# Optimization experiments

Hardware: AMD Instinct MI355X
Metric: run time of the kernel (lower is better)

## Reference

```python
import jax, jax.numpy as jnp
import numpy as np

N_USERS = 30000
N_ENT = 70000
N = N_USERS + N_ENT          # total graph nodes
E = 1_600_000                # edges (avg degree 16)
D = 64                       # embed_dim
B = 4096                     # scored user-item pairs
LEAKY_SLOPE = 0.01           # torch nn.LeakyReLU default
EPS = 1e-12                  # torch F.normalize default eps


def setup_inputs() -> dict:
    key = jax.random.key(0)
    ks = jax.random.split(key, 16)
    inp = {
        "edge_row": jax.random.randint(ks[0], (E,), 0, N, dtype=jnp.int32),
        "edge_col": jax.random.randint(ks[1], (E,), 0, N, dtype=jnp.int32),
        "edge_vals": jax.random.uniform(ks[2], (E,), dtype=jnp.float32) / 16.0,
        "user_embed": jax.random.normal(ks[3], (N_USERS, D), jnp.float32) * 0.1,
        "entity_embed": jax.random.normal(ks[4], (N_ENT, D), jnp.float32) * 0.1,
        "W1_0": jax.random.normal(ks[5], (D, 64), jnp.float32) * (1.0 / np.sqrt(D)),
        "b1_0": jnp.zeros((64,), jnp.float32),
        "W2_0": jax.random.normal(ks[6], (D, 64), jnp.float32) * (1.0 / np.sqrt(D)),
        "b2_0": jnp.zeros((64,), jnp.float32),
        "W1_1": jax.random.normal(ks[7], (64, 32), jnp.float32) * (1.0 / 8.0),
        "b1_1": jnp.zeros((32,), jnp.float32),
        "W2_1": jax.random.normal(ks[8], (64, 32), jnp.float32) * (1.0 / 8.0),
        "b2_1": jnp.zeros((32,), jnp.float32),
        "user_ids": jax.random.randint(ks[9], (B,), 0, N_USERS, dtype=jnp.int32),
        "item_ids": jax.random.randint(ks[10], (B,), 0, N_ENT, dtype=jnp.int32),
    }
    return inp


def _gnn_layer(feats, edge_row, edge_col, edge_vals, W1, b1, W2, b2):
    # sparse adj @ feats  ==  scatter-add of weighted source features to rows
    gathered = feats[edge_col] * edge_vals[:, None]          # (E, d_in)
    h_neigh = jax.ops.segment_sum(gathered, edge_row, num_segments=N)  # (N, d_in)
    term1 = (feats + h_neigh) @ W1 + b1
    term2 = (feats * h_neigh) @ W2 + b2
    h = jax.nn.leaky_relu(term1 + term2, negative_slope=LEAKY_SLOPE)
    # F.normalize(h, p=2, dim=1)
    norm = jnp.linalg.norm(h, axis=1, keepdims=True)
    return h / jnp.maximum(norm, EPS)


def reference(edge_row, edge_col, edge_vals, user_embed, entity_embed,
              W1_0, b1_0, W2_0, b2_0, W1_1, b1_1, W2_1, b2_1,
              user_ids, item_ids):
    a0 = jnp.concatenate([user_embed, entity_embed], axis=0)     # (N, 64)
    a1 = _gnn_layer(a0, edge_row, edge_col, edge_vals, W1_0, b1_0, W2_0, b2_0)  # (N, 64)
    a2 = _gnn_layer(a1, edge_row, edge_col, edge_vals, W1_1, b1_1, W2_1, b2_1)  # (N, 32)
    final = jnp.concatenate([a0, a1, a2], axis=1)                # (N, 160)
    u = final[user_ids]                                          # (B, 160)
    i = final[N_USERS + item_ids]                                # (B, 160)
    return jnp.sum(u * i, axis=1)                                # (B,)
```

## Files before the change

kernel.cpp:

```cpp
#include <hip/hip_runtime.h>
#include <hip/hip_bf16.h>
#include <math.h>

#define LEAKY 0.01f
#define SCAN_BLOCK 256
#define SCAN_ITEMS 4
#define SCAN_TILE (SCAN_BLOCK * SCAN_ITEMS)

struct __align__(8) Bf4 { __hip_bfloat16 a, b, c, d; };

__global__ void zero_i32(int* __restrict__ p, int n) {
    int i = blockIdx.x * blockDim.x + threadIdx.x;
    if (i < n) p[i] = 0;
}

__global__ void count_edges(const int* __restrict__ row, int E,
                            int* __restrict__ deg, int* __restrict__ rank) {
    int i = blockIdx.x * blockDim.x + threadIdx.x;
    if (i < E) rank[i] = atomicAdd(&deg[row[i]], 1);
}

__global__ __launch_bounds__(SCAN_BLOCK) void scan_phase1(
    const int* __restrict__ deg, int* __restrict__ blocksum, int N) {
    __shared__ int red[SCAN_BLOCK];
    int b = blockIdx.x, t = threadIdx.x;
    int base = b * SCAN_TILE + t * SCAN_ITEMS;
    int s = 0;
#pragma unroll
    for (int j = 0; j < SCAN_ITEMS; j++) {
        int i = base + j;
        if (i < N) s += deg[i];
    }
    red[t] = s;
    __syncthreads();
    for (int off = SCAN_BLOCK / 2; off > 0; off >>= 1) {
        if (t < off) red[t] += red[t + off];
        __syncthreads();
    }
    if (t == 0) blocksum[b] = red[0];
}

__global__ __launch_bounds__(1024) void scan_phase2(
    const int* __restrict__ blocksum, int* __restrict__ blockoff,
    int* __restrict__ row_ptr, int G, int N) {
    __shared__ int sums[1024];
    int t = threadIdx.x;
    sums[t] = (t < G) ? blocksum[t] : 0;
    __syncthreads();
    for (int off = 1; off < 1024; off <<= 1) {
        int v = (t >= off) ? sums[t - off] : 0;
        __syncthreads();
        sums[t] += v;
        __syncthreads();
    }
    if (t < G) blockoff[t] = (t == 0) ? 0 : sums[t - 1];
    if (t == G - 1) row_ptr[N] = sums[t];
}

__global__ __launch_bounds__(SCAN_BLOCK) void scan_phase3(
    const int* __restrict__ deg, const int* __restrict__ blockoff,
    int* __restrict__ row_ptr, int N) {
    __shared__ int red[SCAN_BLOCK];
    int b = blockIdx.x, t = threadIdx.x;
    int base = b * SCAN_TILE + t * SCAN_ITEMS;
    int v[SCAN_ITEMS];
    int s = 0;
#pragma unroll
    for (int j = 0; j < SCAN_ITEMS; j++) {
        int i = base + j;
        v[j] = (i < N) ? deg[i] : 0;
        s += v[j];
    }
    red[t] = s;
    __syncthreads();
    for (int off = 1; off < SCAN_BLOCK; off <<= 1) {
        int x = (t >= off) ? red[t - off] : 0;
        __syncthreads();
        red[t] += x;
        __syncthreads();
    }
    int run = blockoff[b] + ((t == 0) ? 0 : red[t - 1]);
#pragma unroll
    for (int j = 0; j < SCAN_ITEMS; j++) {
        int i = base + j;
        if (i < N) { row_ptr[i] = run; run += v[j]; }
    }
}

__global__ void build_a0(const float4* __restrict__ ue, const float4* __restrict__ ee,
                         float4* __restrict__ a0, __hip_bfloat16* __restrict__ a0b,
                         int nu4, int ntot4) {
    int i = blockIdx.x * blockDim.x + threadIdx.x;
    if (i < ntot4) {
        float4 v = (i < nu4) ? ue[i] : ee[i - nu4];
        a0[i] = v;
        Bf4 q = {__float2bfloat16(v.x), __float2bfloat16(v.y),
                 __float2bfloat16(v.z), __float2bfloat16(v.w)};
        *(Bf4*)&a0b[(size_t)i * 4] = q;
    }
}

__global__ void fill_csr(const int* __restrict__ row, const int* __restrict__ col,
                         const float* __restrict__ val, const int* __restrict__ rank,
                         const int* __restrict__ row_ptr, int E,
                         int2* __restrict__ csr) {
    int i = blockIdx.x * blockDim.x + threadIdx.x;
    if (i < E) {
        int p = row_ptr[row[i]] + rank[i];
        csr[p] = make_int2(col[i], __float_as_int(val[i]));
    }
}

__device__ __forceinline__ void fma4(float o[4], float sv, const float4& wv) {
    o[0] = fmaf(sv, wv.x, o[0]);
    o[1] = fmaf(sv, wv.y, o[1]);
    o[2] = fmaf(sv, wv.z, o[2]);
    o[3] = fmaf(sv, wv.w, o[3]);
}

template<int DOUT>
__global__ __launch_bounds__(256, 8) void gnn_layer(
    const float* __restrict__ feats, const __hip_bfloat16* __restrict__ featsb,
    const int2* __restrict__ csr, const int* __restrict__ row_ptr,
    const float* __restrict__ W1, const float* __restrict__ b1,
    const float* __restrict__ W2, const float* __restrict__ b2,
    float* __restrict__ out, __hip_bfloat16* __restrict__ outb, int N) {
    __shared__ __align__(16) float S[32 * 132];
    int wv = threadIdx.x >> 6, lane = threadIdx.x & 63;
    int nb = blockIdx.x * 32 + wv * 8;

    for (int ni = 0; ni < 8; ni++) {
        int node = nb + ni;
        if (node >= N) break;
        int e0   = __builtin_amdgcn_readfirstlane(row_ptr[node]);
        int e1   = __builtin_amdgcn_readfirstlane(row_ptr[node + 1]);
        int degn = e1 - e0;
        float x = feats[(size_t)node * 64 + lane];
        float acc = 0.f;
        for (int g = 0; g < degn; g += 16) {
            float fv[16], vv[16];
#pragma unroll
            for (int u = 0; u < 16; u++) {
                int j = g + u;
                bool live = (j < degn);
                int2 e = csr[e0 + (live ? j : 0)];
                vv[u] = live ? __int_as_float(e.y) : 0.f;
                fv[u] = __bfloat162float(featsb[(size_t)e.x * 64 + lane]);
            }
#pragma unroll
            for (int u = 0; u < 16; u++) acc = fmaf(vv[u], fv[u], acc);
        }
        float* sp = &S[(wv * 8 + ni) * 132];
        sp[lane]      = x + acc;
        sp[64 + lane] = x * acc;
    }
    __threadfence_block();

    if constexpr (DOUT == 64) {
        int strip = lane & 15, g = lane >> 4;
        int d0 = strip * 4;
        float4 b1v = *(const float4*)&b1[d0];
        float4 b2v = *(const float4*)&b2[d0];
        float oa[4] = {b1v.x + b2v.x, b1v.y + b2v.y, b1v.z + b2v.z, b1v.w + b2v.w};
        float ob[4] = {oa[0], oa[1], oa[2], oa[3]};
        const float* spa = &S[(wv * 8 + 2 * g) * 132];
        const float* spb = spa + 132;
#pragma unroll
        for (int half = 0; half < 2; half++) {
            const float* W  = half ? W2 : W1;
            const float* sa = spa + half * 64;
            const float* sb = spb + half * 64;
#pragma unroll 2
            for (int k = 0; k < 64; k += 4) {
                float4 va = *(const float4*)&sa[k];
                float4 vb = *(const float4*)&sb[k];
                float4 wr0 = *(const float4*)&W[(k + 0) * 64 + d0];
                float4 wr1 = *(const float4*)&W[(k + 1) * 64 + d0];
                float4 wr2 = *(const float4*)&W[(k + 2) * 64 + d0];
                float4 wr3 = *(const float4*)&W[(k + 3) * 64 + d0];
                fma4(oa, va.x, wr0); fma4(oa, va.y, wr1);
                fma4(oa, va.z, wr2); fma4(oa, va.w, wr3);
                fma4(ob, vb.x, wr0); fma4(ob, vb.y, wr1);
                fma4(ob, vb.z, wr2); fma4(ob, vb.w, wr3);
            }
        }
#pragma unroll
        for (int t = 0; t < 2; t++) {
            float* o = t ? ob : oa;
            float h0 = (o[0] > 0.f) ? o[0] : LEAKY * o[0];
            float h1 = (o[1] > 0.f) ? o[1] : LEAKY * o[1];
            float h2 = (o[2] > 0.f) ? o[2] : LEAKY * o[2];
            float h3 = (o[3] > 0.f) ? o[3] : LEAKY * o[3];
            float ss = h0 * h0 + h1 * h1 + h2 * h2 + h3 * h3;
            ss += __shfl_xor(ss, 1, 64);
            ss += __shfl_xor(ss, 2, 64);
            ss += __shfl_xor(ss, 4, 64);
            ss += __shfl_xor(ss, 8, 64);
            float sc = 1.0f / fmaxf(sqrtf(ss), 1e-12f);
            int node = nb + 2 * g + t;
            if (node < N) {
                float4 r = {h0 * sc, h1 * sc, h2 * sc, h3 * sc};
                *(float4*)&out[(size_t)node * 64 + d0] = r;
                Bf4 q = {__float2bfloat16(r.x), __float2bfloat16(r.y),
                         __float2bfloat16(r.z), __float2bfloat16(r.w)};
                *(Bf4*)&outb[(size_t)node * 64 + d0] = q;
            }
        }
    } else {
        int strip = lane & 7, nI = lane >> 3;
        int d0 = strip * 4;
        float4 b1v = *(const float4*)&b1[d0];
        float4 b2v = *(const float4*)&b2[d0];
        float o[4] = {b1v.x + b2v.x, b1v.y + b2v.y, b1v.z + b2v.z, b1v.w + b2v.w};
        const float* sp = &S[(wv * 8 + nI) * 132];
#pragma unroll
        for (int half = 0; half < 2; half++) {
            const float* W  = half ? W2 : W1;
            const float* sv = sp + half * 64;
#pragma unroll 2
            for (int k = 0; k < 64; k += 4) {
                float4 v   = *(const float4*)&sv[k];
                float4 wr0 = *(const float4*)&W[(k + 0) * 32 + d0];
                float4 wr1 = *(const float4*)&W[(k + 1) * 32 + d0];
                float4 wr2 = *(const float4*)&W[(k + 2) * 32 + d0];
                float4 wr3 = *(const float4*)&W[(k + 3) * 32 + d0];
                fma4(o, v.x, wr0); fma4(o, v.y, wr1);
                fma4(o, v.z, wr2); fma4(o, v.w, wr3);
            }
        }
        float h0 = (o[0] > 0.f) ? o[0] : LEAKY * o[0];
        float h1 = (o[1] > 0.f) ? o[1] : LEAKY * o[1];
        float h2 = (o[2] > 0.f) ? o[2] : LEAKY * o[2];
        float h3 = (o[3] > 0.f) ? o[3] : LEAKY * o[3];
        float ss = h0 * h0 + h1 * h1 + h2 * h2 + h3 * h3;
        ss += __shfl_xor(ss, 1, 64);
        ss += __shfl_xor(ss, 2, 64);
        ss += __shfl_xor(ss, 4, 64);
        float sc = 1.0f / fmaxf(sqrtf(ss), 1e-12f);
        int node = nb + nI;
        if (node < N) {
            float4 r = {h0 * sc, h1 * sc, h2 * sc, h3 * sc};
            *(float4*)&out[(size_t)node * 32 + d0] = r;
        }
    }
}

__global__ __launch_bounds__(256) void score_pairs(
    const float* __restrict__ a0, const float* __restrict__ a1,
    const float* __restrict__ a2,
    const int* __restrict__ uid, const int* __restrict__ iid,
    float* __restrict__ out, int B, int NU) {
    int wave = threadIdx.x >> 6, lane = threadIdx.x & 63;
    int p = blockIdx.x * 4 + wave;
    if (p >= B) return;
    int u = uid[p], it = iid[p];
    size_t un = (size_t)u, in = (size_t)(NU + it);
    float s = a0[un * 64 + lane] * a0[in * 64 + lane];
    s = fmaf(a1[un * 64 + lane], a1[in * 64 + lane], s);
    if (lane < 32) s = fmaf(a2[un * 32 + lane], a2[in * 32 + lane], s);
#pragma unroll
    for (int m = 32; m >= 1; m >>= 1) s += __shfl_xor(s, m, 64);
    if (lane == 0) out[p] = s;
}

extern "C" void kernel_launch(void* const* d_in, const int* in_sizes, int n_in,
                              void* d_out, int out_size, void* d_ws, size_t ws_size,
                              hipStream_t stream) {
    const int*   edge_row  = (const int*)d_in[0];
    const int*   edge_col  = (const int*)d_in[1];
    const float* edge_vals = (const float*)d_in[2];
    const float* ue        = (const float*)d_in[3];
    const float* ee        = (const float*)d_in[4];
    const float* W1_0 = (const float*)d_in[5];
    const float* b1_0 = (const float*)d_in[6];
    const float* W2_0 = (const float*)d_in[7];
    const float* b2_0 = (const float*)d_in[8];
    const float* W1_1 = (const float*)d_in[9];
    const float* b1_1 = (const float*)d_in[10];
    const float* W2_1 = (const float*)d_in[11];
    const float* b2_1 = (const float*)d_in[12];
    const int*   uid  = (const int*)d_in[13];
    const int*   iid  = (const int*)d_in[14];
    float* out = (float*)d_out;

    const int E  = in_sizes[0];
    const int NU = in_sizes[3] / 64;
    const int NE = in_sizes[4] / 64;
    const int N  = NU + NE;
    const int B  = in_sizes[13];
    const int G  = (N + SCAN_TILE - 1) / SCAN_TILE;

    char* ws = (char*)d_ws;
    size_t off = 0;
    auto alloc = [&](size_t bytes) -> char* {
        char* p = ws + off;
        off = (off + bytes + 255) & ~(size_t)255;
        return p;
    };
    int*   deg      = (int*)alloc((size_t)N * 4);
    int*   rank     = (int*)alloc((size_t)E * 4);
    int*   row_ptr  = (int*)alloc((size_t)(N + 1) * 4);
    int*   blocksum = (int*)alloc((size_t)1024 * 4);
    int*   blockoff = (int*)alloc((size_t)1024 * 4);
    int2*  csr      = (int2*)alloc((size_t)E * 8);
    float* a0       = (float*)alloc((size_t)N * 64 * 4);
    float* a1       = (float*)alloc((size_t)N * 64 * 4);
    float* a2       = (float*)alloc((size_t)N * 32 * 4);
    __hip_bfloat16* a0b = (__hip_bfloat16*)alloc((size_t)N * 64 * 2);
    __hip_bfloat16* a1b = (__hip_bfloat16*)alloc((size_t)N * 64 * 2);
    (void)ws_size; (void)n_in; (void)out_size; (void)NE;

    zero_i32<<<(N + 255) / 256, 256, 0, stream>>>(deg, N);
    count_edges<<<(E + 255) / 256, 256, 0, stream>>>(edge_row, E, deg, rank);
    scan_phase1<<<G, SCAN_BLOCK, 0, stream>>>(deg, blocksum, N);
    scan_phase2<<<1, 1024, 0, stream>>>(blocksum, blockoff, row_ptr, G, N);
    scan_phase3<<<G, SCAN_BLOCK, 0, stream>>>(deg, blockoff, row_ptr, N);
    fill_csr<<<(E + 255) / 256, 256, 0, stream>>>(edge_row, edge_col, edge_vals,
                                                  rank, row_ptr, E, csr);
    int ntot4 = N * 16, nu4 = NU * 16;
    build_a0<<<(ntot4 + 255) / 256, 256, 0, stream>>>((const float4*)ue, (const float4*)ee,
                                                      (float4*)a0, a0b, nu4, ntot4);
    gnn_layer<64><<<(N + 31) / 32, 256, 0, stream>>>(a0, a0b, csr, row_ptr,
                                                     W1_0, b1_0, W2_0, b2_0, a1, a1b, N);
    gnn_layer<32><<<(N + 31) / 32, 256, 0, stream>>>(a1, a1b, csr, row_ptr,
                                                     W1_1, b1_1, W2_1, b2_1, a2, nullptr, N);
    score_pairs<<<(B + 3) / 4, 256, 0, stream>>>(a0, a1, a2, uid, iid, out, B, NU);
}
```

Before: 417.4 us.

## Software-pipeline neighbor gathers across nodes with double-buffered register banks

```diff
diff --git a/kernel.cpp b/kernel.cpp
--- a/kernel.cpp
+++ b/kernel.cpp
@@ -118,42 +118,117 @@
     o[3] = fmaf(sv, wv.w, o[3]);
 }
 
+#define ISSUE(BANK, K) do {                                                   \
+    int dn_ = min(dg[K], 32);                                                 \
+    _Pragma("unroll")                                                         \
+    for (int c_ = 0; c_ < 4; c_++) {                                          \
+        if (c_ * 8 < dn_) {                                                   \
+            _Pragma("unroll")                                                 \
+            for (int u_ = 0; u_ < 8; u_++) {                                  \
+                int j_ = min(c_ * 8 + u_, dn_ - 1);                           \
+                int col_ = __shfl(m[K].x, j_, 64);                            \
+                BANK[c_ * 8 + u_] =                                           \
+                    __bfloat162float(featsb[(size_t)col_ * 64 + lane]);       \
+            }                                                                 \
+        }                                                                     \
+    }                                                                         \
+} while (0)
+
+#define CONSUME(BANK, K) do {                                                 \
+    float acc_ = 0.f;                                                         \
+    int dn_ = min(dg[K], 32);                                                 \
+    _Pragma("unroll")                                                         \
+    for (int c_ = 0; c_ < 4; c_++) {                                          \
+        if (c_ * 8 < dn_) {                                                   \
+            _Pragma("unroll")                                                 \
+            for (int u_ = 0; u_ < 8; u_++) {                                  \
+                int j_ = c_ * 8 + u_;                                         \
+                float vv_ = (j_ < dn_)                                        \
+                    ? __int_as_float(__shfl(m[K].y, j_, 64)) : 0.f;           \
+                acc_ = fmaf(vv_, BANK[c_ * 8 + u_], acc_);                    \
+            }                                                                 \
+        }                                                                     \
+    }                                                                         \
+    if (dg[K] > 32) {       \
+        int dm_ = min(dg[K], 64);                                             \
+        for (int j_ = 32; j_ < dm_; j_++) {                                   \
+            int col_ = __shfl(m[K].x, j_, 64);                                \
+            float vv_ = __int_as_float(__shfl(m[K].y, j_, 64));               \
+            acc_ = fmaf(vv_,                                                  \
+                __bfloat162float(featsb[(size_t)col_ * 64 + lane]), acc_);    \
+        }                                                                     \
+    }                                                                         \
+    if (dg[K] > 64) {                  \
+        for (int done_ = 64; done_ < dg[K]; done_ += 64) {                    \
+            int take_ = min(64, dg[K] - done_);                               \
+            int2 mm_ = csr[min(e0[K] + done_ + min(lane, take_ - 1), Em1)];   \
+            for (int g_ = 0; g_ < take_; g_ += 8) {                           \
+                _Pragma("unroll")                                             \
+                for (int u_ = 0; u_ < 8; u_++) {                              \
+                    int j_ = g_ + u_;                                         \
+                    float vt_ = (j_ < take_)                                  \
+                        ? __int_as_float(__shfl(mm_.y, j_, 64)) : 0.f;        \
+                    int cl_ = __shfl(mm_.x, min(j_, take_ - 1), 64);          \
+                    acc_ = fmaf(vt_,                                          \
+                        __bfloat162float(featsb[(size_t)cl_ * 64 + lane]),    \
+                        acc_);                                                \
+                }                                                             \
+            }                                                                 \
+        }                                                                     \
+    }                                                                         \
+    if (nb + K < N) {                                                         \
+        float* sp_ = &S[(wv * 8 + K) * 132];                                  \
+        sp_[lane]      = x[K] + acc_;                                         \
+        sp_[64 + lane] = x[K] * acc_;                                         \
+    }                                                                         \
+} while (0)
+
 template<int DOUT>
-__global__ __launch_bounds__(256, 8) void gnn_layer(
+__global__ __launch_bounds__(256, 4) void gnn_layer(
     const float* __restrict__ feats, const __hip_bfloat16* __restrict__ featsb,
     const int2* __restrict__ csr, const int* __restrict__ row_ptr,
     const float* __restrict__ W1, const float* __restrict__ b1,
     const float* __restrict__ W2, const float* __restrict__ b2,
-    float* __restrict__ out, __hip_bfloat16* __restrict__ outb, int N) {
+    float* __restrict__ out, __hip_bfloat16* __restrict__ outb, int N, int E) {
     __shared__ __align__(16) float S[32 * 132];
     int wv = threadIdx.x >> 6, lane = threadIdx.x & 63;
     int nb = blockIdx.x * 32 + wv * 8;
-
+    int Em1 = E - 1;
+
+    int rp_l = row_ptr[min(nb + min(lane, 8), N)];
+    int e0[8], dg[8];
+#pragma unroll
     for (int ni = 0; ni < 8; ni++) {
-        int node = nb + ni;
-        if (node >= N) break;
-        int e0   = __builtin_amdgcn_readfirstlane(row_ptr[node]);
-        int e1   = __builtin_amdgcn_readfirstlane(row_ptr[node + 1]);
-        int degn = e1 - e0;
-        float x = feats[(size_t)node * 64 + lane];
-        float acc = 0.f;
-        for (int g = 0; g < degn; g += 16) {
-            float fv[16], vv[16];
-#pragma unroll
-            for (int u = 0; u < 16; u++) {
-                int j = g + u;
-                bool live = (j < degn);
-                int2 e = csr[e0 + (live ? j : 0)];
-                vv[u] = live ? __int_as_float(e.y) : 0.f;
-                fv[u] = __bfloat162float(featsb[(size_t)e.x * 64 + lane]);
-            }
-#pragma unroll
-            for (int u = 0; u < 16; u++) acc = fmaf(vv[u], fv[u], acc);
-        }
-        float* sp = &S[(wv * 8 + ni) * 132];
-        sp[lane]      = x + acc;
-        sp[64 + lane] = x * acc;
-    }
+        int a = __builtin_amdgcn_readlane(rp_l, ni);
+        int b = __builtin_amdgcn_readlane(rp_l, ni + 1);
+        e0[ni] = a; dg[ni] = b - a;
+    }
+    float x[8];
+    int2 m[8];
+#pragma unroll
+    for (int ni = 0; ni < 8; ni++) {
+        int node = min(nb + ni, N - 1);
+        x[ni] = feats[(size_t)node * 64 + lane];
+        m[ni] = csr[min(e0[ni] + lane, Em1)];
+    }
+
+    float fvA[32], fvB[32];
+    ISSUE(fvA, 0);
+    ISSUE(fvB, 1);
+    CONSUME(fvA, 0);
+    ISSUE(fvA, 2);
+    CONSUME(fvB, 1);
+    ISSUE(fvB, 3);
+    CONSUME(fvA, 2);
+    ISSUE(fvA, 4);
+    CONSUME(fvB, 3);
+    ISSUE(fvB, 5);
+    CONSUME(fvA, 4);
+    ISSUE(fvA, 6);
+    CONSUME(fvB, 5);
+    ISSUE(fvB, 7);
+    CONSUME(fvA, 6);
+    CONSUME(fvB, 7);
     __threadfence_block();
 
     if constexpr (DOUT == 64) {
@@ -321,8 +396,8 @@
     build_a0<<<(ntot4 + 255) / 256, 256, 0, stream>>>((const float4*)ue, (const float4*)ee,
                                                       (float4*)a0, a0b, nu4, ntot4);
     gnn_layer<64><<<(N + 31) / 32, 256, 0, stream>>>(a0, a0b, csr, row_ptr,
-                                                     W1_0, b1_0, W2_0, b2_0, a1, a1b, N);
+                                                     W1_0, b1_0, W2_0, b2_0, a1, a1b, N, E);
     gnn_layer<32><<<(N + 31) / 32, 256, 0, stream>>>(a1, a1b, csr, row_ptr,
-                                                     W1_1, b1_1, W2_1, b2_1, a2, nullptr, N);
+                                                     W1_1, b1_1, W2_1, b2_1, a2, nullptr, N, E);
     score_pairs<<<(B + 3) / 4, 256, 0, stream>>>(a0, a1, a2, uid, iid, out, B, NU);
 }
```

Result: slower. 437.4 us (+4.8%).

## Process two nodes per wavefront with coalesced CSR loads and lane shuffles

Applied to the files above, without the earlier changes.

```diff
diff --git a/kernel.cpp b/kernel.cpp
--- a/kernel.cpp
+++ b/kernel.cpp
@@ -8,11 +8,6 @@
 #define SCAN_TILE (SCAN_BLOCK * SCAN_ITEMS)
 
 struct __align__(8) Bf4 { __hip_bfloat16 a, b, c, d; };
-
-__global__ void zero_i32(int* __restrict__ p, int n) {
-    int i = blockIdx.x * blockDim.x + threadIdx.x;
-    if (i < n) p[i] = 0;
-}
 
 __global__ void count_edges(const int* __restrict__ row, int E,
                             int* __restrict__ deg, int* __restrict__ rank) {
@@ -128,31 +123,55 @@
     __shared__ __align__(16) float S[32 * 132];
     int wv = threadIdx.x >> 6, lane = threadIdx.x & 63;
     int nb = blockIdx.x * 32 + wv * 8;
-
+    int sl = lane & 31;
+    int selbase = lane & 32;
+
+    int rp_l = row_ptr[min(nb + min(lane, 8), N)];
+    int e0[8], dg[8];
+#pragma unroll
     for (int ni = 0; ni < 8; ni++) {
-        int node = nb + ni;
-        if (node >= N) break;
-        int e0   = __builtin_amdgcn_readfirstlane(row_ptr[node]);
-        int e1   = __builtin_amdgcn_readfirstlane(row_ptr[node + 1]);
-        int degn = e1 - e0;
-        float x = feats[(size_t)node * 64 + lane];
-        float acc = 0.f;
-        for (int g = 0; g < degn; g += 16) {
-            float fv[16], vv[16];
-#pragma unroll
-            for (int u = 0; u < 16; u++) {
-                int j = g + u;
-                bool live = (j < degn);
-                int2 e = csr[e0 + (live ? j : 0)];
-                vv[u] = live ? __int_as_float(e.y) : 0.f;
-                fv[u] = __bfloat162float(featsb[(size_t)e.x * 64 + lane]);
+        int a = __builtin_amdgcn_readlane(rp_l, ni);
+        int b = __builtin_amdgcn_readlane(rp_l, ni + 1);
+        e0[ni] = a; dg[ni] = b - a;
+    }
+
+    const uint* fb2 = (const uint*)featsb;
+    const float2* f2 = (const float2*)feats;
+
+#pragma unroll
+    for (int pr = 0; pr < 4; pr++) {
+        int nA = nb + 2 * pr, nB = nA + 1;
+        int myNode = selbase ? nB : nA;
+        int myE0   = selbase ? e0[2 * pr + 1] : e0[2 * pr];
+        int myDg   = selbase ? dg[2 * pr + 1] : dg[2 * pr];
+        int mx = max(dg[2 * pr], dg[2 * pr + 1]);
+        float2 x = f2[(size_t)min(myNode, N - 1) * 32 + sl];
+        float accx = 0.f, accy = 0.f;
+        for (int done = 0; done < mx; done += 32) {
+            int2 m = make_int2(0, 0);
+            if (sl < myDg - done) m = csr[myE0 + done + sl];
+            int lim = min(mx - done, 32);
+            for (int c = 0; c < lim; c += 8) {
+                uint w[8]; float vv[8];
+#pragma unroll
+                for (int u = 0; u < 8; u++) {
+                    int j = c + u;
+                    int col = __shfl(m.x, selbase + j, 64);
+                    vv[u] = __int_as_float(__shfl(m.y, selbase + j, 64));
+                    w[u] = fb2[(size_t)col * 32 + sl];
+                }
+#pragma unroll
+                for (int u = 0; u < 8; u++) {
+                    accx = fmaf(vv[u], __uint_as_float(w[u] << 16), accx);
+                    accy = fmaf(vv[u], __uint_as_float(w[u] & 0xffff0000u), accy);
+                }
             }
-#pragma unroll
-            for (int u = 0; u < 16; u++) acc = fmaf(vv[u], fv[u], acc);
-        }
-        float* sp = &S[(wv * 8 + ni) * 132];
-        sp[lane]      = x + acc;
-        sp[64 + lane] = x * acc;
+        }
+        if (myNode < N) {
+            float* sp = &S[(wv * 8 + 2 * pr + (selbase ? 1 : 0)) * 132];
+            *(float2*)&sp[2 * sl]      = make_float2(x.x + accx, x.y + accy);
+            *(float2*)&sp[64 + 2 * sl] = make_float2(x.x * accx, x.y * accy);
+        }
     }
     __threadfence_block();
 
@@ -310,7 +329,7 @@
     __hip_bfloat16* a1b = (__hip_bfloat16*)alloc((size_t)N * 64 * 2);
     (void)ws_size; (void)n_in; (void)out_size; (void)NE;
 
-    zero_i32<<<(N + 255) / 256, 256, 0, stream>>>(deg, N);
+    hipMemsetAsync(deg, 0, (size_t)N * 4, stream);
     count_edges<<<(E + 255) / 256, 256, 0, stream>>>(edge_row, E, deg, rank);
     scan_phase1<<<G, SCAN_BLOCK, 0, stream>>>(deg, blocksum, N);
     scan_phase2<<<1, 1024, 0, stream>>>(blocksum, blockoff, row_ptr, G, N);
```

New measurement: 393.8 us. 5.6% less time.
